# Performance work log

Hardware: AMD Instinct MI355X
Metric: run time of the kernel (lower is better)

The kernel has to match this reference:

```python
import jax, jax.numpy as jnp
import numpy as np

N, E, D, H = 4096, 131072, 256, 8
HD = D // H
NEG_INF = -1e30  # stand-in for float('-inf'); avoids inf-inf NaN issues, softmax identical


def _linear(x, W, b):
    return x @ W + b


def setup_inputs() -> dict:
    key = jax.random.key(0)
    ks = jax.random.split(key, 16)
    s = 1.0 / np.sqrt(D)
    inp = {
        "x": jax.random.normal(ks[0], (N, D), jnp.float32),
        "edge_index": jax.random.randint(ks[1], (2, E), 0, N, jnp.int32),
        "edge_attr": jax.random.normal(ks[2], (E, D), jnp.float32),
        "Wq": jax.random.normal(ks[3], (D, D), jnp.float32) * s,
        "bq": jnp.zeros((D,), jnp.float32),
        "Wk": jax.random.normal(ks[4], (D, D), jnp.float32) * s,
        "bk": jnp.zeros((D,), jnp.float32),
        "Wv": jax.random.normal(ks[5], (D, D), jnp.float32) * s,
        "bv": jnp.zeros((D,), jnp.float32),
        "We": jax.random.normal(ks[6], (D, D), jnp.float32) * s,
        "be": jnp.zeros((D,), jnp.float32),
        "Wo": jax.random.normal(ks[7], (D, D), jnp.float32) * s,
        "bo": jnp.zeros((D,), jnp.float32),
        "Wi": jax.random.normal(ks[8], (D, D), jnp.float32) * s,
        "bi": jnp.zeros((D,), jnp.float32),
        "ln_g": jnp.ones((D,), jnp.float32),
        "ln_b": jnp.zeros((D,), jnp.float32),
    }
    return inp


def reference(x, edge_index, edge_attr, Wq, bq, Wk, bk, Wv, bv, We, be, Wo, bo, Wi, bi, ln_g, ln_b):
    n, e = x.shape[0], edge_attr.shape[0]
    Q = _linear(x, Wq, bq).reshape(n, H, HD)
    K = _linear(x, Wk, bk).reshape(n, H, HD)
    V = _linear(x, Wv, bv).reshape(n, H, HD)
    Efeat = _linear(edge_attr, We, be).reshape(e, H, HD)

    src, tgt = edge_index[0], edge_index[1]
    Q_src = Q[src]                     # (E, H, HD)
    K_tgt = K[tgt]                     # (E, H, HD)
    attn_edge = ((Q_src * K_tgt).sum(-1)
                 + (Q_src * Efeat).sum(-1)
                 + (Efeat * K_tgt).sum(-1)) / np.sqrt(HD)   # (E, H)

    attn_scores = jnp.full((n, n, H), NEG_INF, jnp.float32)
    attn_scores = attn_scores.at[src, tgt].set(attn_edge)
    attn_self = (Q * K).sum(-1) / np.sqrt(HD)               # (N, H)
    ar = jnp.arange(n)
    attn_scores = attn_scores.at[ar, ar].set(attn_self)

    attn_weights = jax.nn.softmax(attn_scores, axis=1)      # (N, N, H)
    # dropout in eval mode: identity
    node_out = jnp.einsum('ijh,jhd->ihd', attn_weights, V).reshape(n, -1)
    node_out = _linear(node_out, Wo, bo)

    x_proj = _linear(x, Wi, bi)
    h = x_proj + node_out
    mu = h.mean(-1, keepdims=True)
    var = ((h - mu) ** 2).mean(-1, keepdims=True)
    node_out = (h - mu) / jnp.sqrt(var + 1e-5) * ln_g + ln_b

    edge_out = _linear(edge_attr, We, be)
    return node_out, edge_out
```

## Files before the change

### kernel.cpp

```cpp
#include <hip/hip_runtime.h>

#define N_NODES 4096
#define N_EDGES 131072
#define DIM     256
#define HEADS   8
#define HDIM    32
#define MAXDEG  320
#define MAXDEGP 321

typedef unsigned short u16;
typedef unsigned int   u32;

using f32x4  = __attribute__((ext_vector_type(4))) float;
using bf16x8 = __attribute__((ext_vector_type(8))) short;
using u16x4  = __attribute__((ext_vector_type(4))) unsigned short;
using u16x8  = __attribute__((ext_vector_type(8))) unsigned short;

__device__ __forceinline__ u16 f2bf(float f) {
  u32 u = __float_as_uint(f);
  u += 0x7fffu + ((u >> 16) & 1u);
  return (u16)(u >> 16);
}

__device__ __forceinline__ float dot4(float4 a, float4 b) {
  return a.x * b.x + a.y * b.y + a.z * b.z + a.w * b.w;
}

__global__ __launch_bounds__(256) void prep_w_k(
    const float* __restrict__ Wq, const float* __restrict__ Wk,
    const float* __restrict__ Wv, const float* __restrict__ Wi,
    const float* __restrict__ We, const float* __restrict__ Wo,
    const float* __restrict__ bq, const float* __restrict__ bk,
    const float* __restrict__ bv, const float* __restrict__ bi,
    u16* __restrict__ WcatT, u16* __restrict__ WeT, u16* __restrict__ WoT,
    float* __restrict__ bcat, int* __restrict__ deg)
{
  int n = blockIdx.x;
  int k = threadIdx.x;
  if (n < 1024) {
    const float* W = (n < 256) ? Wq : (n < 512) ? Wk : (n < 768) ? Wv : Wi;
    int nn = n & 255;
    WcatT[(size_t)n * 256 + k] = f2bf(W[(size_t)k * 256 + nn]);
    if (k == 0) {
      const float* b = (n < 256) ? bq : (n < 512) ? bk : (n < 768) ? bv : bi;
      bcat[n] = b[nn];
    }
  } else if (n < 1280) {
    int nn = n - 1024;
    WeT[(size_t)nn * 256 + k] = f2bf(We[(size_t)k * 256 + nn]);
  } else if (n < 1536) {
    int nn = n - 1280;
    WoT[(size_t)nn * 256 + k] = f2bf(Wo[(size_t)k * 256 + nn]);
  } else {
    deg[(n - 1536) * 256 + k] = 0;
  }
}

__device__ __forceinline__ void gemm_big_body(
    const float* __restrict__ A, const u16* __restrict__ BT,
    const float* __restrict__ bias, float* __restrict__ C, int Nn,
    int m0, int nc0, u16 (&As)[2][128 * 32], u16 (&Bs)[2][256 * 32])
{
  const int tid = threadIdx.x;
  const int w = tid >> 6, l = tid & 63;
  const int wr = w >> 2, wc = w & 3;
  const int fr = l & 15, hi = l >> 4;

  f32x4 pa[2];
  u16x8 pb[2];
  f32x4 acc[4][4] = {};

  auto loadstep = [&](int kt) {
#pragma unroll
    for (int i = 0; i < 2; ++i) {
      int j = tid + 512 * i;
      pa[i] = __builtin_nontemporal_load(
          (const f32x4*)(A + (size_t)(m0 + (j >> 3)) * 256 + kt * 32 + ((j & 7) << 2)));
    }
#pragma unroll
    for (int i = 0; i < 2; ++i) {
      int j = tid + 512 * i;
      pb[i] = *(const u16x8*)(BT + (size_t)(nc0 + (j >> 2)) * 256 + kt * 32 + ((j & 3) << 3));
    }
  };
  auto storestep = [&](int buf) {
#pragma unroll
    for (int i = 0; i < 2; ++i) {
      int j = tid + 512 * i;
      int row = j >> 3;
      int c16 = (j & 7) >> 1, half = j & 1;
      int swc = (c16 + ((row >> 1) & 3)) & 3;
      u16x4 u;
      u.x = f2bf(pa[i][0]); u.y = f2bf(pa[i][1]); u.z = f2bf(pa[i][2]); u.w = f2bf(pa[i][3]);
      *(u16x4*)&As[buf][row * 32 + swc * 8 + half * 4] = u;
    }
#pragma unroll
    for (int i = 0; i < 2; ++i) {
      int j = tid + 512 * i;
      int row = j >> 2;
      int swc = ((j & 3) + ((row >> 1) & 3)) & 3;
      *(u16x8*)&Bs[buf][row * 32 + swc * 8] = pb[i];
    }
  };

  loadstep(0);
  storestep(0);

#pragma unroll
  for (int kt = 0; kt < 8; ++kt) {
    if (kt < 7) loadstep(kt + 1);
    __builtin_amdgcn_sched_barrier(0);
    asm volatile("s_waitcnt lgkmcnt(0)" ::: "memory");
    __builtin_amdgcn_s_barrier();
    __builtin_amdgcn_sched_barrier(0);
    const int cur = kt & 1;
    bf16x8 a[4], b[4];
#pragma unroll
    for (int mi = 0; mi < 4; ++mi) {
      int rA = wr * 64 + mi * 16 + fr;
      int swc = (hi + ((rA >> 1) & 3)) & 3;
      a[mi] = *(const bf16x8*)&As[cur][rA * 32 + swc * 8];
    }
#pragma unroll
    for (int ni = 0; ni < 4; ++ni) {
      int rB = wc * 64 + ni * 16 + fr;
      int swc = (hi + ((rB >> 1) & 3)) & 3;
      b[ni] = *(const bf16x8*)&Bs[cur][rB * 32 + swc * 8];
    }
#pragma unroll
    for (int mi = 0; mi < 4; ++mi)
#pragma unroll
      for (int ni = 0; ni < 4; ++ni)
        acc[mi][ni] = __builtin_amdgcn_mfma_f32_16x16x32_bf16(
            b[ni], a[mi], acc[mi][ni], 0, 0, 0);
    if (kt < 7) storestep((kt + 1) & 1);
  }

#pragma unroll
  for (int mi = 0; mi < 4; ++mi) {
    int row = m0 + wr * 64 + mi * 16 + fr;
#pragma unroll
    for (int ni = 0; ni < 4; ++ni) {
      int col = nc0 + wc * 64 + ni * 16 + hi * 4;
      float4 bv = *(const float4*)&bias[col];
      f32x4 v = acc[mi][ni];
      float4 o;
      o.x = v[0] + bv.x; o.y = v[1] + bv.y; o.z = v[2] + bv.z; o.w = v[3] + bv.w;
      *(float4*)&C[(size_t)row * Nn + col] = o;
    }
  }
}

__global__ __launch_bounds__(512) void gemm_all_k(
    const float* __restrict__ ea, const u16* __restrict__ WeT,
    const float* __restrict__ be, float* __restrict__ outE,
    const float* __restrict__ x, const u16* __restrict__ WcatT,
    const float* __restrict__ bcat, float* __restrict__ QKVI)
{
  __shared__ u16 As[2][128 * 32];
  __shared__ u16 Bs[2][256 * 32];
  int bid = blockIdx.x;
  int r = bid % 9, q = bid / 9;
  if (r < 8) {
    int j = q * 8 + r;
    gemm_big_body(ea, WeT, be, outE, 256, j * 128, 0, As, Bs);
  } else {
    gemm_big_body(x, WcatT, bcat, QKVI, 1024, (q >> 2) * 128, (q & 3) * 256, As, Bs);
  }
}

__global__ __launch_bounds__(512) void gemm_wo_k(
    const float* __restrict__ agg, const u16* __restrict__ WoT,
    const float* __restrict__ bo, float* __restrict__ preo)
{
  __shared__ u16 As[2][128 * 32];
  __shared__ u16 Bs[2][256 * 32];
  gemm_big_body(agg, WoT, bo, preo, 256, blockIdx.x * 128, 0, As, Bs);
}

__global__ __launch_bounds__(256) void hist_k(const int* __restrict__ src, int* __restrict__ deg)
{
  int e = blockIdx.x * 256 + threadIdx.x;
  if (e < N_EDGES) atomicAdd(&deg[src[e]], 1);
}

__global__ __launch_bounds__(1024) void scan_k(const int* __restrict__ deg,
                                               int* __restrict__ rowstart,
                                               int* __restrict__ cursor)
{
  __shared__ int s[1024];
  int tid = threadIdx.x;
  int4 v = ((const int4*)deg)[tid];
  int sum = v.x + v.y + v.z + v.w;
  s[tid] = sum;
  __syncthreads();
  for (int off = 1; off < 1024; off <<= 1) {
    int t = (tid >= off) ? s[tid - off] : 0;
    __syncthreads();
    s[tid] += t;
    __syncthreads();
  }
  int excl = s[tid] - sum;
  int r0 = excl, r1 = excl + v.x, r2 = r1 + v.y, r3 = r2 + v.z;
  rowstart[4 * tid + 0] = r0; cursor[4 * tid + 0] = r0;
  rowstart[4 * tid + 1] = r1; cursor[4 * tid + 1] = r1;
  rowstart[4 * tid + 2] = r2; cursor[4 * tid + 2] = r2;
  rowstart[4 * tid + 3] = r3; cursor[4 * tid + 3] = r3;
  if (tid == 1023) rowstart[4096] = r3 + v.w;
}

__global__ __launch_bounds__(256) void scatter_k(const int* __restrict__ src,
                                                 int* __restrict__ cursor,
                                                 int* __restrict__ csr)
{
  int e = blockIdx.x * 256 + threadIdx.x;
  if (e < N_EDGES) {
    int p = atomicAdd(&cursor[src[e]], 1);
    csr[p] = e;
  }
}

__global__ __launch_bounds__(256) void node_attn_k(
    const float* __restrict__ QKVI, const float* __restrict__ Ef,
    const int* __restrict__ rowstart, const int* __restrict__ csr,
    const int* __restrict__ tgt, float* __restrict__ agg)
{
  __shared__ int   s_eid[MAXDEG];
  __shared__ int   s_tgt[MAXDEG];
  __shared__ float s_sc[HEADS][MAXDEGP];
  __shared__ unsigned char s_alive[MAXDEG];
  __shared__ float s_self[8];
  __shared__ float s_wself[8];

  const float scl = 0.17677669529663687f;
  int i = blockIdx.x;
  int base = rowstart[i];
  int deg = rowstart[i + 1] - base;
  if (deg > MAXDEG) deg = MAXDEG;
  int tid = threadIdx.x;
  int w = tid >> 6, l = tid & 63;
  int h = tid >> 5, d = tid & 31;

  for (int t = tid; t < deg; t += 256) {
    int e = csr[base + t];
    s_eid[t] = e;
    s_tgt[t] = tgt[e];
  }
  __syncthreads();

  float4 q4 = *(const float4*)&QKVI[(size_t)i * 1024 + 4 * l];

  if (w == 0) {
    float4 k4 = *(const float4*)&QKVI[(size_t)i * 1024 + 256 + 4 * l];
    float c = dot4(q4, k4);
    c += __shfl_xor(c, 1); c += __shfl_xor(c, 2); c += __shfl_xor(c, 4);
    if ((l & 7) == 0) s_self[l >> 3] = c * scl;
  }

  for (int t0 = w; t0 < deg; t0 += 16) {
    float4 ef[4], k4[4];
#pragma unroll
    for (int u = 0; u < 4; ++u) {
      int t = t0 + 4 * u;
      if (t < deg) {
        ef[u] = *(const float4*)&Ef[(size_t)s_eid[t] * 256 + 4 * l];
        k4[u] = *(const float4*)&QKVI[(size_t)s_tgt[t] * 1024 + 256 + 4 * l];
      }
    }
#pragma unroll
    for (int u = 0; u < 4; ++u) {
      int t = t0 + 4 * u;
      if (t < deg) {
        float c = dot4(q4, ef[u]) + dot4(ef[u], k4[u]) + dot4(q4, k4[u]);
        c += __shfl_xor(c, 1); c += __shfl_xor(c, 2); c += __shfl_xor(c, 4);
        if ((l & 7) == 0) s_sc[l >> 3][t] = c * scl;
      }
    }
  }

  for (int t = tid; t < deg; t += 256) {
    int tt = s_tgt[t], ee = s_eid[t];
    bool alive = (tt != i);
    if (alive)
      for (int u = 0; u < deg; ++u)
        if (s_tgt[u] == tt && s_eid[u] > ee) { alive = false; break; }
    s_alive[t] = alive ? 1 : 0;
  }
  __syncthreads();

  {
    float m = s_self[h];
    for (int t = d; t < deg; t += 32)
      if (s_alive[t]) m = fmaxf(m, s_sc[h][t]);
#pragma unroll
    for (int off = 16; off > 0; off >>= 1) m = fmaxf(m, __shfl_xor(m, off, 32));
    float lsum = 0.f;
    for (int t = d; t < deg; t += 32) {
      float wv = s_alive[t] ? expf(s_sc[h][t] - m) : 0.f;
      s_sc[h][t] = wv;
      lsum += wv;
    }
#pragma unroll
    for (int off = 16; off > 0; off >>= 1) lsum += __shfl_xor(lsum, off, 32);
    float wself = expf(s_self[h] - m);
    float inv = 1.f / (lsum + wself);
    if (d == 0) s_wself[h] = wself * inv;
    for (int t = d; t < deg; t += 32) s_sc[h][t] *= inv;
  }
  __syncthreads();

  int col = tid;
  float accv = s_wself[h] * QKVI[(size_t)i * 1024 + 512 + col];
  int t0 = 0;
  for (; t0 + 4 <= deg; t0 += 4) {
    float vl[4];
#pragma unroll
    for (int u = 0; u < 4; ++u)
      vl[u] = QKVI[(size_t)s_tgt[t0 + u] * 1024 + 512 + col];
#pragma unroll
    for (int u = 0; u < 4; ++u)
      accv += s_sc[h][t0 + u] * vl[u];
  }
  for (; t0 < deg; ++t0)
    accv += s_sc[h][t0] * QKVI[(size_t)s_tgt[t0] * 1024 + 512 + col];
  agg[(size_t)i * 256 + col] = accv;
}

__global__ __launch_bounds__(256) void ln_k(
    const float* __restrict__ QKVI, const float* __restrict__ preo,
    const float* __restrict__ g, const float* __restrict__ b,
    float* __restrict__ out)
{
  int i = blockIdx.x, c = threadIdx.x;
  float v = QKVI[(size_t)i * 1024 + 768 + c] + preo[(size_t)i * 256 + c];
  float s1 = v, s2 = v * v;
#pragma unroll
  for (int off = 32; off > 0; off >>= 1) {
    s1 += __shfl_xor(s1, off, 64);
    s2 += __shfl_xor(s2, off, 64);
  }
  __shared__ float r1[4], r2[4];
  int w = c >> 6;
  if ((c & 63) == 0) { r1[w] = s1; r2[w] = s2; }
  __syncthreads();
  s1 = r1[0] + r1[1] + r1[2] + r1[3];
  s2 = r2[0] + r2[1] + r2[2] + r2[3];
  float mu  = s1 * (1.0f / 256.0f);
  float var = s2 * (1.0f / 256.0f) - mu * mu;
  out[(size_t)i * 256 + c] = (v - mu) * rsqrtf(var + 1e-5f) * g[c] + b[c];
}

extern "C" void kernel_launch(void* const* d_in, const int* in_sizes, int n_in,
                              void* d_out, int out_size, void* d_ws, size_t ws_size,
                              hipStream_t stream) {
  (void)in_sizes; (void)n_in; (void)out_size; (void)ws_size;
  const float* x  = (const float*)d_in[0];
  const int*   ei = (const int*)d_in[1];
  const float* ea = (const float*)d_in[2];
  const float* Wq = (const float*)d_in[3];  const float* bq = (const float*)d_in[4];
  const float* Wk = (const float*)d_in[5];  const float* bk = (const float*)d_in[6];
  const float* Wv = (const float*)d_in[7];  const float* bv = (const float*)d_in[8];
  const float* We = (const float*)d_in[9];  const float* be = (const float*)d_in[10];
  const float* Wo = (const float*)d_in[11]; const float* bo = (const float*)d_in[12];
  const float* Wi = (const float*)d_in[13]; const float* bi = (const float*)d_in[14];
  const float* lng = (const float*)d_in[15]; const float* lnb = (const float*)d_in[16];

  const int* src = ei;
  const int* tgt = ei + N_EDGES;

  char* ws = (char*)d_ws;
  u16*   WcatT   = (u16*)(ws + 0);
  u16*   WeT     = (u16*)(ws + 524288);
  u16*   WoT     = (u16*)(ws + 655360);
  float* bcat    = (float*)(ws + 786432);
  float* QKVI    = (float*)(ws + 790528);
  int*   deg     = (int*)(ws + 17567744);
  int*   rowstart= (int*)(ws + 17584128);
  int*   cursor  = (int*)(ws + 17600768);
  int*   csr     = (int*)(ws + 17617152);
  float* agg     = (float*)(ws + 18141440);
  float* preo    = (float*)(ws + 22335744);

  float* outN = (float*)d_out;
  float* outE = (float*)d_out + (size_t)N_NODES * DIM;

  prep_w_k<<<1552, 256, 0, stream>>>(Wq, Wk, Wv, Wi, We, Wo, bq, bk, bv, bi,
                                     WcatT, WeT, WoT, bcat, deg);

  hist_k<<<N_EDGES / 256, 256, 0, stream>>>(src, deg);
  scan_k<<<1, 1024, 0, stream>>>(deg, rowstart, cursor);
  scatter_k<<<N_EDGES / 256, 256, 0, stream>>>(src, cursor, csr);

  gemm_all_k<<<1152, 512, 0, stream>>>(ea, WeT, be, outE, x, WcatT, bcat, QKVI);

  node_attn_k<<<N_NODES, 256, 0, stream>>>(QKVI, outE, rowstart, csr, tgt, agg);

  gemm_wo_k<<<N_NODES / 128, 512, 0, stream>>>(agg, WoT, bo, preo);

  ln_k<<<N_NODES, 256, 0, stream>>>(QKVI, preo, lng, lnb, outN);
}
```

Baseline: 175.8 us.

## Store bf16 K/V and CSR-ordered edge features; fuse LayerNorm into Wo GEMM

The QKV GEMM epilogue now also writes compact bf16 copies of K and V. When the workspace is large enough, the edge GEMM epilogue also writes a bf16 copy of the edge features permuted into CSR order, using a new per-edge position array filled by the scatter kernel. The attention kernel reads these half-size, contiguous streams instead of scattered fp32 rows, cutting gather traffic. The Wo GEMM epilogue now computes the residual add and LayerNorm itself, which removes the separate ln_k launch and the preo round trip. The costs are extra bf16 writes in the GEMMs, reduced precision for K, V and edge features in the scores, and a dependence on ws_size for the edge-feature path.

```diff
diff --git a/kernel.cpp b/kernel.cpp
--- a/kernel.cpp
+++ b/kernel.cpp
@@ -7,6 +7,7 @@
 #define HDIM    32
 #define MAXDEG  320
 #define MAXDEGP 321
+#define WS_EFB_BYTES 94163200ull
 
 typedef unsigned short u16;
 typedef unsigned int   u32;
@@ -21,7 +22,9 @@
   u += 0x7fffu + ((u >> 16) & 1u);
   return (u16)(u >> 16);
 }
-
+__device__ __forceinline__ float bf2f(u16 u) {
+  return __uint_as_float(((u32)u) << 16);
+}
 __device__ __forceinline__ float dot4(float4 a, float4 b) {
   return a.x * b.x + a.y * b.y + a.z * b.z + a.w * b.w;
 }
@@ -56,10 +59,16 @@
   }
 }
 
+template<int MODE, bool EFB>
 __device__ __forceinline__ void gemm_big_body(
     const float* __restrict__ A, const u16* __restrict__ BT,
     const float* __restrict__ bias, float* __restrict__ C, int Nn,
-    int m0, int nc0, u16 (&As)[2][128 * 32], u16 (&Bs)[2][256 * 32])
+    int m0, int nc0,
+    const int* __restrict__ epos, u16* __restrict__ EfCSR,
+    u16* __restrict__ Kb, u16* __restrict__ Vb,
+    const float* __restrict__ QKVI, const float* __restrict__ lng,
+    const float* __restrict__ lnb, float* __restrict__ outN,
+    u16 (&As)[2][128 * 32], u16 (&Bs)[2][256 * 32])
 {
   const int tid = threadIdx.x;
   const int w = tid >> 6, l = tid & 63;
@@ -136,26 +145,114 @@
     if (kt < 7) storestep((kt + 1) & 1);
   }
 
-#pragma unroll
-  for (int mi = 0; mi < 4; ++mi) {
-    int row = m0 + wr * 64 + mi * 16 + fr;
-#pragma unroll
-    for (int ni = 0; ni < 4; ++ni) {
-      int col = nc0 + wc * 64 + ni * 16 + hi * 4;
-      float4 bv = *(const float4*)&bias[col];
-      f32x4 v = acc[mi][ni];
-      float4 o;
-      o.x = v[0] + bv.x; o.y = v[1] + bv.y; o.z = v[2] + bv.z; o.w = v[3] + bv.w;
-      *(float4*)&C[(size_t)row * Nn + col] = o;
-    }
-  }
-}
-
+  if constexpr (MODE == 0) {
+#pragma unroll
+    for (int mi = 0; mi < 4; ++mi) {
+      int row = m0 + wr * 64 + mi * 16 + fr;
+      int p = 0;
+      if (EFB) p = epos[row];
+#pragma unroll
+      for (int ni = 0; ni < 4; ++ni) {
+        int col = wc * 64 + ni * 16 + hi * 4;
+        float4 bv = *(const float4*)&bias[col];
+        f32x4 v = acc[mi][ni];
+        float4 o;
+        o.x = v[0] + bv.x; o.y = v[1] + bv.y; o.z = v[2] + bv.z; o.w = v[3] + bv.w;
+        *(float4*)&C[(size_t)row * 256 + col] = o;
+        if (EFB) {
+          u16x4 ub;
+          ub.x = f2bf(o.x); ub.y = f2bf(o.y); ub.z = f2bf(o.z); ub.w = f2bf(o.w);
+          *(u16x4*)&EfCSR[(size_t)p * 256 + col] = ub;
+        }
+      }
+    }
+  } else if constexpr (MODE == 1) {
+#pragma unroll
+    for (int mi = 0; mi < 4; ++mi) {
+      int row = m0 + wr * 64 + mi * 16 + fr;
+#pragma unroll
+      for (int ni = 0; ni < 4; ++ni) {
+        int col = nc0 + wc * 64 + ni * 16 + hi * 4;
+        float4 bv = *(const float4*)&bias[col];
+        f32x4 v = acc[mi][ni];
+        float4 o;
+        o.x = v[0] + bv.x; o.y = v[1] + bv.y; o.z = v[2] + bv.z; o.w = v[3] + bv.w;
+        *(float4*)&C[(size_t)row * 1024 + col] = o;
+        u16x4 ub;
+        ub.x = f2bf(o.x); ub.y = f2bf(o.y); ub.z = f2bf(o.z); ub.w = f2bf(o.w);
+        if (nc0 == 256) *(u16x4*)&Kb[(size_t)row * 256 + (col - 256)] = ub;
+        if (nc0 == 512) *(u16x4*)&Vb[(size_t)row * 256 + (col - 512)] = ub;
+      }
+    }
+  } else {
+    __syncthreads();
+    float* s_sum = (float*)&As[0][0];
+    float* s_sq  = (float*)&As[1][0];
+#pragma unroll
+    for (int mi = 0; mi < 4; ++mi) {
+      int r = wr * 64 + mi * 16 + fr;
+      int row = m0 + r;
+      float ps = 0.f, pq = 0.f;
+#pragma unroll
+      for (int ni = 0; ni < 4; ++ni) {
+        int col = wc * 64 + ni * 16 + hi * 4;
+        float4 bv = *(const float4*)&bias[col];
+        float4 xp = *(const float4*)&QKVI[(size_t)row * 1024 + 768 + col];
+        acc[mi][ni][0] += bv.x + xp.x;
+        acc[mi][ni][1] += bv.y + xp.y;
+        acc[mi][ni][2] += bv.z + xp.z;
+        acc[mi][ni][3] += bv.w + xp.w;
+#pragma unroll
+        for (int j = 0; j < 4; ++j) {
+          float vv = acc[mi][ni][j];
+          ps += vv; pq += vv * vv;
+        }
+      }
+      s_sum[r * 16 + wc * 4 + hi] = ps;
+      s_sq [r * 16 + wc * 4 + hi] = pq;
+    }
+    __syncthreads();
+    float* s_mu = (float*)&Bs[0][0];
+    float* s_rs = s_mu + 128;
+    if (tid < 128) {
+      float s = 0.f, q = 0.f;
+#pragma unroll
+      for (int k = 0; k < 16; ++k) { s += s_sum[tid * 16 + k]; q += s_sq[tid * 16 + k]; }
+      float mu = s * (1.0f / 256.0f);
+      float var = q * (1.0f / 256.0f) - mu * mu;
+      s_mu[tid] = mu;
+      s_rs[tid] = rsqrtf(var + 1e-5f);
+    }
+    __syncthreads();
+#pragma unroll
+    for (int mi = 0; mi < 4; ++mi) {
+      int r = wr * 64 + mi * 16 + fr;
+      int row = m0 + r;
+      float mu = s_mu[r], rs = s_rs[r];
+#pragma unroll
+      for (int ni = 0; ni < 4; ++ni) {
+        int col = wc * 64 + ni * 16 + hi * 4;
+        float4 g4 = *(const float4*)&lng[col];
+        float4 b4 = *(const float4*)&lnb[col];
+        float4 o;
+        o.x = (acc[mi][ni][0] - mu) * rs * g4.x + b4.x;
+        o.y = (acc[mi][ni][1] - mu) * rs * g4.y + b4.y;
+        o.z = (acc[mi][ni][2] - mu) * rs * g4.z + b4.z;
+        o.w = (acc[mi][ni][3] - mu) * rs * g4.w + b4.w;
+        *(float4*)&outN[(size_t)row * 256 + col] = o;
+      }
+    }
+  }
+}
+
+template<bool EFB>
 __global__ __launch_bounds__(512) void gemm_all_k(
     const float* __restrict__ ea, const u16* __restrict__ WeT,
     const float* __restrict__ be, float* __restrict__ outE,
     const float* __restrict__ x, const u16* __restrict__ WcatT,
-    const float* __restrict__ bcat, float* __restrict__ QKVI)
+    const float* __restrict__ bcat, float* __restrict__ QKVI,
+    const int* __restrict__ epos, u16* __restrict__ EfCSR,
+    u16* __restrict__ Kb, u16* __restrict__ Vb)
 {
   __shared__ u16 As[2][128 * 32];
   __shared__ u16 Bs[2][256 * 32];
@@ -163,19 +260,24 @@
   int r = bid % 9, q = bid / 9;
   if (r < 8) {
     int j = q * 8 + r;
-    gemm_big_body(ea, WeT, be, outE, 256, j * 128, 0, As, Bs);
+    gemm_big_body<0, EFB>(ea, WeT, be, outE, 256, j * 128, 0,
+                          epos, EfCSR, Kb, Vb, nullptr, nullptr, nullptr, nullptr, As, Bs);
   } else {
-    gemm_big_body(x, WcatT, bcat, QKVI, 1024, (q >> 2) * 128, (q & 3) * 256, As, Bs);
+    gemm_big_body<1, EFB>(x, WcatT, bcat, QKVI, 1024, (q >> 2) * 128, (q & 3) * 256,
+                          nullptr, nullptr, Kb, Vb, nullptr, nullptr, nullptr, nullptr, As, Bs);
   }
 }
 
 __global__ __launch_bounds__(512) void gemm_wo_k(
     const float* __restrict__ agg, const u16* __restrict__ WoT,
-    const float* __restrict__ bo, float* __restrict__ preo)
+    const float* __restrict__ bo, const float* __restrict__ QKVI,
+    const float* __restrict__ lng, const float* __restrict__ lnb,
+    float* __restrict__ outN)
 {
   __shared__ u16 As[2][128 * 32];
   __shared__ u16 Bs[2][256 * 32];
-  gemm_big_body(agg, WoT, bo, preo, 256, blockIdx.x * 128, 0, As, Bs);
+  gemm_big_body<2, false>(agg, WoT, bo, nullptr, 256, blockIdx.x * 128, 0,
+                          nullptr, nullptr, nullptr, nullptr, QKVI, lng, lnb, outN, As, Bs);
 }
 
 __global__ __launch_bounds__(256) void hist_k(const int* __restrict__ src, int* __restrict__ deg)
@@ -211,17 +313,22 @@
 
 __global__ __launch_bounds__(256) void scatter_k(const int* __restrict__ src,
                                                  int* __restrict__ cursor,
-                                                 int* __restrict__ csr)
+                                                 int* __restrict__ csr,
+                                                 int* __restrict__ epos)
 {
   int e = blockIdx.x * 256 + threadIdx.x;
   if (e < N_EDGES) {
     int p = atomicAdd(&cursor[src[e]], 1);
     csr[p] = e;
-  }
-}
-
+    epos[e] = p;
+  }
+}
+
+template<bool EFB>
 __global__ __launch_bounds__(256) void node_attn_k(
     const float* __restrict__ QKVI, const float* __restrict__ Ef,
+    const u16* __restrict__ EfCSR, const u16* __restrict__ Kb,
+    const u16* __restrict__ Vb,
     const int* __restrict__ rowstart, const int* __restrict__ csr,
     const int* __restrict__ tgt, float* __restrict__ agg)
 {
@@ -251,7 +358,8 @@
   float4 q4 = *(const float4*)&QKVI[(size_t)i * 1024 + 4 * l];
 
   if (w == 0) {
-    float4 k4 = *(const float4*)&QKVI[(size_t)i * 1024 + 256 + 4 * l];
+    u16x4 kb = *(const u16x4*)&Kb[(size_t)i * 256 + 4 * l];
+    float4 k4 = make_float4(bf2f(kb.x), bf2f(kb.y), bf2f(kb.z), bf2f(kb.w));
     float c = dot4(q4, k4);
     c += __shfl_xor(c, 1); c += __shfl_xor(c, 2); c += __shfl_xor(c, 4);
     if ((l & 7) == 0) s_self[l >> 3] = c * scl;
@@ -263,8 +371,14 @@
     for (int u = 0; u < 4; ++u) {
       int t = t0 + 4 * u;
       if (t < deg) {
-        ef[u] = *(const float4*)&Ef[(size_t)s_eid[t] * 256 + 4 * l];
-        k4[u] = *(const float4*)&QKVI[(size_t)s_tgt[t] * 1024 + 256 + 4 * l];
+        if (EFB) {
+          u16x4 ub = *(const u16x4*)&EfCSR[(size_t)(base + t) * 256 + 4 * l];
+          ef[u] = make_float4(bf2f(ub.x), bf2f(ub.y), bf2f(ub.z), bf2f(ub.w));
+        } else {
+          ef[u] = *(const float4*)&Ef[(size_t)s_eid[t] * 256 + 4 * l];
+        }
+        u16x4 kb = *(const u16x4*)&Kb[(size_t)s_tgt[t] * 256 + 4 * l];
+        k4[u] = make_float4(bf2f(kb.x), bf2f(kb.y), bf2f(kb.z), bf2f(kb.w));
       }
     }
 #pragma unroll
@@ -310,50 +424,26 @@
   __syncthreads();
 
   int col = tid;
-  float accv = s_wself[h] * QKVI[(size_t)i * 1024 + 512 + col];
+  float accv = s_wself[h] * bf2f(Vb[(size_t)i * 256 + col]);
   int t0 = 0;
   for (; t0 + 4 <= deg; t0 += 4) {
     float vl[4];
 #pragma unroll
     for (int u = 0; u < 4; ++u)
-      vl[u] = QKVI[(size_t)s_tgt[t0 + u] * 1024 + 512 + col];
+      vl[u] = bf2f(Vb[(size_t)s_tgt[t0 + u] * 256 + col]);
 #pragma unroll
     for (int u = 0; u < 4; ++u)
       accv += s_sc[h][t0 + u] * vl[u];
   }
   for (; t0 < deg; ++t0)
-    accv += s_sc[h][t0] * QKVI[(size_t)s_tgt[t0] * 1024 + 512 + col];
+    accv += s_sc[h][t0] * bf2f(Vb[(size_t)s_tgt[t0] * 256 + col]);
   agg[(size_t)i * 256 + col] = accv;
-}
-
-__global__ __launch_bounds__(256) void ln_k(
-    const float* __restrict__ QKVI, const float* __restrict__ preo,
-    const float* __restrict__ g, const float* __restrict__ b,
-    float* __restrict__ out)
-{
-  int i = blockIdx.x, c = threadIdx.x;
-  float v = QKVI[(size_t)i * 1024 + 768 + c] + preo[(size_t)i * 256 + c];
-  float s1 = v, s2 = v * v;
-#pragma unroll
-  for (int off = 32; off > 0; off >>= 1) {
-    s1 += __shfl_xor(s1, off, 64);
-    s2 += __shfl_xor(s2, off, 64);
-  }
-  __shared__ float r1[4], r2[4];
-  int w = c >> 6;
-  if ((c & 63) == 0) { r1[w] = s1; r2[w] = s2; }
-  __syncthreads();
-  s1 = r1[0] + r1[1] + r1[2] + r1[3];
-  s2 = r2[0] + r2[1] + r2[2] + r2[3];
-  float mu  = s1 * (1.0f / 256.0f);
-  float var = s2 * (1.0f / 256.0f) - mu * mu;
-  out[(size_t)i * 256 + c] = (v - mu) * rsqrtf(var + 1e-5f) * g[c] + b[c];
 }
 
 extern "C" void kernel_launch(void* const* d_in, const int* in_sizes, int n_in,
                               void* d_out, int out_size, void* d_ws, size_t ws_size,
                               hipStream_t stream) {
-  (void)in_sizes; (void)n_in; (void)out_size; (void)ws_size;
+  (void)in_sizes; (void)n_in; (void)out_size;
   const float* x  = (const float*)d_in[0];
   const int*   ei = (const int*)d_in[1];
   const float* ea = (const float*)d_in[2];
@@ -378,24 +468,37 @@
   int*   rowstart= (int*)(ws + 17584128);
   int*   cursor  = (int*)(ws + 17600768);
   int*   csr     = (int*)(ws + 17617152);
-  float* agg     = (float*)(ws + 18141440);
-  float* preo    = (float*)(ws + 22335744);
+  int*   epos    = (int*)(ws + 18141440);
+  float* agg     = (float*)(ws + 18665728);
+  u16*   Kb      = (u16*)(ws + 22860032);
+  u16*   Vb      = (u16*)(ws + 24957184);
+  u16*   EfCSR   = (u16*)(ws + 27054336);
 
   float* outN = (float*)d_out;
   float* outE = (float*)d_out + (size_t)N_NODES * DIM;
 
+  const bool efb = ws_size >= WS_EFB_BYTES;
+
   prep_w_k<<<1552, 256, 0, stream>>>(Wq, Wk, Wv, Wi, We, Wo, bq, bk, bv, bi,
                                      WcatT, WeT, WoT, bcat, deg);
 
   hist_k<<<N_EDGES / 256, 256, 0, stream>>>(src, deg);
   scan_k<<<1, 1024, 0, stream>>>(deg, rowstart, cursor);
-  scatter_k<<<N_EDGES / 256, 256, 0, stream>>>(src, cursor, csr);
-
-  gemm_all_k<<<1152, 512, 0, stream>>>(ea, WeT, be, outE, x, WcatT, bcat, QKVI);
-
-  node_attn_k<<<N_NODES, 256, 0, stream>>>(QKVI, outE, rowstart, csr, tgt, agg);
-
-  gemm_wo_k<<<N_NODES / 128, 512, 0, stream>>>(agg, WoT, bo, preo);
-
-  ln_k<<<N_NODES, 256, 0, stream>>>(QKVI, preo, lng, lnb, outN);
-}
+  scatter_k<<<N_EDGES / 256, 256, 0, stream>>>(src, cursor, csr, epos);
+
+  if (efb)
+    gemm_all_k<true><<<1152, 512, 0, stream>>>(ea, WeT, be, outE, x, WcatT, bcat,
+                                               QKVI, epos, EfCSR, Kb, Vb);
+  else
+    gemm_all_k<false><<<1152, 512, 0, stream>>>(ea, WeT, be, outE, x, WcatT, bcat,
+                                                QKVI, epos, EfCSR, Kb, Vb);
+
+  if (efb)
+    node_attn_k<true><<<N_NODES, 256, 0, stream>>>(QKVI, outE, EfCSR, Kb, Vb,
+                                                   rowstart, csr, tgt, agg);
+  else
+    node_attn_k<false><<<N_NODES, 256, 0, stream>>>(QKVI, outE, EfCSR, Kb, Vb,
+                                                    rowstart, csr, tgt, agg);
+
+  gemm_wo_k<<<N_NODES / 128, 512, 0, stream>>>(agg, WoT, bo, QKVI, lng, lnb, outN);
+}
```

After: 188.7 us. +7.3%, slower.
